# Performance work log

Measured on AMD Instinct MI355X. Metric: run time of the kernel, lower is better.

## Reference

```python
import jax, jax.numpy as jnp
import numpy as np

TEMPERATURE = 12.5      # EMDLayer temperature
SINKHORN_EPS = 0.05     # entropic regularization for the batched EMD solve
SINKHORN_ITERS = 50     # fixed iteration count (jit-friendly)
WEIGHT_EPS = 1e-05      # OpenCVSolver adds 1e-5 after relu


def setup_inputs() -> dict:
    key = jax.random.key(0)
    k1, k2, k3 = jax.random.split(key, 3)
    E, Q, W, N = 4, 75, 5, 64
    similarity_map = jax.random.uniform(k1, (E, Q, W, N, N), dtype=jnp.float32)
    weight_1 = jax.random.uniform(k2, (E, Q, W, N), dtype=jnp.float32)
    weight_2 = jax.random.uniform(k3, (E, W, Q, N), dtype=jnp.float32)
    return {"similarity_map": similarity_map, "weight_1": weight_1, "weight_2": weight_2}


def _emd_flow(cost, a, b):
    """Batched entropic-regularized EMD (log-domain Sinkhorn).
    cost: [B, N, N]; a, b: [B, N] positive marginals (each sums to N).
    Returns flow: [B, N, N] with row sums ~a and col sums ~b."""
    logK = -cost / SINKHORN_EPS            # [B, N, N]
    log_a = jnp.log(a)
    log_b = jnp.log(b)

    def step(carry, _):
        log_u, log_v = carry
        log_u = log_a - jax.scipy.special.logsumexp(logK + log_v[:, None, :], axis=2)
        log_v = log_b - jax.scipy.special.logsumexp(logK + log_u[:, :, None], axis=1)
        return (log_u, log_v), None

    init = (jnp.zeros_like(log_a), jnp.zeros_like(log_b))
    (log_u, log_v), _ = jax.lax.scan(step, init, None, length=SINKHORN_ITERS)
    return jnp.exp(logK + log_u[:, :, None] + log_v[:, None, :])


def reference(similarity_map, weight_1, weight_2):
    E, Q, W, N, _ = similarity_map.shape
    sim = similarity_map.reshape(-1, N, N)                       # [B, N, N]
    w1 = weight_1.reshape(-1, N)                                  # [B, N]
    w2 = jnp.transpose(weight_2, (0, 2, 1, 3)).reshape(-1, N)     # transpose(1,2) then flatten

    # OpenCVSolver weight preprocessing: relu + eps, renormalize to sum N
    w1 = jax.nn.relu(w1) + WEIGHT_EPS
    w1 = w1 * (N / jnp.sum(w1, axis=1, keepdims=True))
    w2 = jax.nn.relu(w2) + WEIGHT_EPS
    w2 = w2 * (N / jnp.sum(w2, axis=1, keepdims=True))

    cost = 1.0 - sim
    flow = _emd_flow(cost, w1, w2)                                # [B, N, N]
    scores = jnp.sum(flow * sim, axis=(-1, -2)).reshape(E, Q, W)
    return scores * (TEMPERATURE / N)
```

## Files before the change

kernel.cpp:

```cpp
#include <hip/hip_runtime.h>

#define N 64
#define NPAD 65
#define ITERS 50
#define TEMP 12.5f
#define WEPS 1e-5f
#define QDIM 75
#define WDIM 5

#define ROL(x) __int_as_float(__builtin_amdgcn_update_dpp(0, __float_as_int(x), 0x134, 0xF, 0xF, true))
#define ROR(x) __int_as_float(__builtin_amdgcn_update_dpp(0, __float_as_int(x), 0x13C, 0xF, 0xF, true))

__device__ __forceinline__ float waveReduceSum(float x) {
#pragma unroll
    for (int off = 32; off; off >>= 1) x += __shfl_xor(x, off, 64);
    return x;
}

__global__ __launch_bounds__(64, 1) void emd_systolic(
    const float* __restrict__ sim,
    const float* __restrict__ w1,
    const float* __restrict__ w2,
    float* __restrict__ out,
    int B)
{
    __shared__ float S[N * NPAD];

    const int lane = threadIdx.x;
    const int b    = blockIdx.x;
    const float* gm = sim + (size_t)b * N * N;

    const int dl = (__builtin_amdgcn_update_dpp(0, lane, 0x134, 0xF, 0xF, true) - lane) & 63;
    const int dr = (__builtin_amdgcn_update_dpp(0, lane, 0x13C, 0xF, 0xF, true) - lane) & 63;

    const float4* g4 = (const float4*)gm;
#pragma unroll
    for (int t = 0; t < 16; ++t) {
        float4 x = g4[t * 64 + lane];
        int idx = t * 64 + lane;
        int r = idx >> 4;
        int c = (idx & 15) * 4;
        S[r * NPAD + c + 0] = x.x;
        S[r * NPAD + c + 1] = x.y;
        S[r * NPAD + c + 2] = x.z;
        S[r * NPAD + c + 3] = x.w;
    }
    __syncthreads();

    float KL[32], KR[32], CL[32], CR[32];
#pragma unroll
    for (int m = 0; m < 32; ++m) {
        int cL = (lane + dl * m) & 63;
        int cR = (lane + dr * (m + 1)) & 63;
        KL[m] = __expf((S[lane * NPAD + cL] - 1.0f) * 20.0f);
        KR[m] = __expf((S[lane * NPAD + cR] - 1.0f) * 20.0f);
        CL[m] = __expf((S[cL * NPAD + lane] - 1.0f) * 20.0f);
        CR[m] = __expf((S[cR * NPAD + lane] - 1.0f) * 20.0f);
    }
#pragma unroll
    for (int m = 0; m < 32; ++m) {
        asm volatile("" : "+v"(KL[m]));
        asm volatile("" : "+v"(KR[m]));
        asm volatile("" : "+v"(CL[m]));
        asm volatile("" : "+v"(CR[m]));
    }

    float a_own = w1[(size_t)b * N + lane];
    a_own = fmaxf(a_own, 0.0f) + WEPS;
    a_own *= (float)N / waveReduceSum(a_own);

    const int e  = b / (QDIM * WDIM);
    const int rm = b % (QDIM * WDIM);
    const int q  = rm / WDIM, w = rm % WDIM;
    float b_own = w2[((((size_t)e * WDIM + w) * QDIM) + q) * N + lane];
    b_own = fmaxf(b_own, 0.0f) + WEPS;
    b_own *= (float)N / waveReduceSum(b_own);

    float vv = 1.0f, u = 0.0f;
#pragma unroll 1
    for (int it = 0; it < ITERS; ++it) {
        {
            float wL = vv, wR = vv;
            float accL = KL[0] * wL;
            float accR = 0.0f;
#pragma unroll
            for (int m = 1; m <= 32; ++m) {
                wR = ROR(wR);
                accR = fmaf(KR[m - 1], wR, accR);
                if (m <= 31) {
                    wL = ROL(wL);
                    accL = fmaf(KL[m], wL, accL);
                }
            }
            u = a_own * __builtin_amdgcn_rcpf(accL + accR);
        }
        {
            float wL = u, wR = u;
            float accL = CL[0] * wL;
            float accR = 0.0f;
#pragma unroll
            for (int m = 1; m <= 32; ++m) {
                wR = ROR(wR);
                accR = fmaf(CR[m - 1], wR, accR);
                if (m <= 31) {
                    wL = ROL(wL);
                    accL = fmaf(CL[m], wL, accL);
                }
            }
            vv = b_own * __builtin_amdgcn_rcpf(accL + accR);
        }
    }

    {
        const float cc = 0.69314718056f / 20.0f;
        float wL = vv, wR = vv;
        float sL = KL[0] * fmaf(__log2f(KL[0]), cc, 1.0f) * wL;
        float sR = 0.0f;
#pragma unroll
        for (int m = 1; m <= 32; ++m) {
            wR = ROR(wR);
            sR = fmaf(KR[m - 1] * fmaf(__log2f(KR[m - 1]), cc, 1.0f), wR, sR);
            if (m <= 31) {
                wL = ROL(wL);
                sL = fmaf(KL[m] * fmaf(__log2f(KL[m]), cc, 1.0f), wL, sL);
            }
        }
        float tot = waveReduceSum(u * (sL + sR));
        if (lane == 0) out[b] = tot * (TEMP / (float)N);
    }
}

extern "C" void kernel_launch(void* const* d_in, const int* in_sizes, int n_in,
                              void* d_out, int out_size, void* d_ws, size_t ws_size,
                              hipStream_t stream) {
    const float* sim = (const float*)d_in[0];
    const float* w1  = (const float*)d_in[1];
    const float* w2  = (const float*)d_in[2];
    float* out       = (float*)d_out;
    const int B = in_sizes[0] / (N * N);
    emd_systolic<<<B, 64, 0, stream>>>(sim, w1, w2, out, B);
}
```

Measured before the change: 111.5 us.

## Replace DPP systolic matvec with bf16 MFMA Sinkhorn matvecs via shared memory

Replaces the DPP-rotation register matvec in each Sinkhorn half-step with bf16 MFMA 16x16x32 operations. The kernel matrix and its transpose are held as packed bf16 fragments, and the scaling vector is broadcast through shared memory as the B operand. Only the column of the MFMA result that holds the matvec is used. Per-iteration cost shifts to MFMA issue plus LDS round trips and extra barriers. Storing the kernel matrix in bf16 lowers precision, and the final score now recomputes exp from the shared-memory similarity values.

```diff
diff --git a/kernel.cpp b/kernel.cpp
--- a/kernel.cpp
+++ b/kernel.cpp
@@ -8,8 +8,23 @@
 #define QDIM 75
 #define WDIM 5
 
-#define ROL(x) __int_as_float(__builtin_amdgcn_update_dpp(0, __float_as_int(x), 0x134, 0xF, 0xF, true))
-#define ROR(x) __int_as_float(__builtin_amdgcn_update_dpp(0, __float_as_int(x), 0x13C, 0xF, 0xF, true))
+typedef __attribute__((ext_vector_type(8))) short bf16x8;
+typedef __attribute__((ext_vector_type(4))) float f32x4;
+
+static __device__ __forceinline__ unsigned cvt_pk(float lo, float hi) {
+    unsigned r;
+    asm("v_cvt_pk_bf16_f32 %0, %1, %2" : "=v"(r) : "v"(lo), "v"(hi));
+    return r;
+}
+union FragU { unsigned u[4]; bf16x8 v; };
+static __device__ __forceinline__ bf16x8 pack8(const float e[8]) {
+    FragU f;
+    f.u[0] = cvt_pk(e[0], e[1]);
+    f.u[1] = cvt_pk(e[2], e[3]);
+    f.u[2] = cvt_pk(e[4], e[5]);
+    f.u[3] = cvt_pk(e[6], e[7]);
+    return f.v;
+}
 
 __device__ __forceinline__ float waveReduceSum(float x) {
 #pragma unroll
@@ -17,7 +32,7 @@
     return x;
 }
 
-__global__ __launch_bounds__(64, 1) void emd_systolic(
+__global__ __launch_bounds__(64, 1) void emd_mfma(
     const float* __restrict__ sim,
     const float* __restrict__ w1,
     const float* __restrict__ w2,
@@ -25,13 +40,13 @@
     int B)
 {
     __shared__ float S[N * NPAD];
+    __shared__ __align__(16) float SUM[N], U[N], V[N];
 
     const int lane = threadIdx.x;
     const int b    = blockIdx.x;
+    const int q    = lane >> 4;
+    const int m    = lane & 15;
     const float* gm = sim + (size_t)b * N * N;
-
-    const int dl = (__builtin_amdgcn_update_dpp(0, lane, 0x134, 0xF, 0xF, true) - lane) & 63;
-    const int dr = (__builtin_amdgcn_update_dpp(0, lane, 0x13C, 0xF, 0xF, true) - lane) & 63;
 
     const float4* g4 = (const float4*)gm;
 #pragma unroll
@@ -47,85 +62,112 @@
     }
     __syncthreads();
 
-    float KL[32], KR[32], CL[32], CR[32];
+    bf16x8 KA[4][2], KT[4][2];
 #pragma unroll
-    for (int m = 0; m < 32; ++m) {
-        int cL = (lane + dl * m) & 63;
-        int cR = (lane + dr * (m + 1)) & 63;
-        KL[m] = __expf((S[lane * NPAD + cL] - 1.0f) * 20.0f);
-        KR[m] = __expf((S[lane * NPAD + cR] - 1.0f) * 20.0f);
-        CL[m] = __expf((S[cL * NPAD + lane] - 1.0f) * 20.0f);
-        CR[m] = __expf((S[cR * NPAD + lane] - 1.0f) * 20.0f);
-    }
+    for (int rb = 0; rb < 4; ++rb)
 #pragma unroll
-    for (int m = 0; m < 32; ++m) {
-        asm volatile("" : "+v"(KL[m]));
-        asm volatile("" : "+v"(KR[m]));
-        asm volatile("" : "+v"(CL[m]));
-        asm volatile("" : "+v"(CR[m]));
-    }
+        for (int c = 0; c < 2; ++c) {
+            float e[8];
+            const float* p = &S[(16 * rb + m) * NPAD + 32 * c + 8 * q];
+#pragma unroll
+            for (int j = 0; j < 8; ++j) e[j] = __expf((p[j] - 1.0f) * 20.0f);
+            KA[rb][c] = pack8(e);
+#pragma unroll
+            for (int j = 0; j < 8; ++j)
+                e[j] = __expf((S[(32 * c + 8 * q + j) * NPAD + 16 * rb + m] - 1.0f) * 20.0f);
+            KT[rb][c] = pack8(e);
+        }
+#pragma unroll
+    for (int rb = 0; rb < 4; ++rb)
+#pragma unroll
+        for (int c = 0; c < 2; ++c) {
+            asm volatile("" : "+v"(KA[rb][c]));
+            asm volatile("" : "+v"(KT[rb][c]));
+        }
 
     float a_own = w1[(size_t)b * N + lane];
     a_own = fmaxf(a_own, 0.0f) + WEPS;
     a_own *= (float)N / waveReduceSum(a_own);
 
-    const int e  = b / (QDIM * WDIM);
-    const int rm = b % (QDIM * WDIM);
-    const int q  = rm / WDIM, w = rm % WDIM;
-    float b_own = w2[((((size_t)e * WDIM + w) * QDIM) + q) * N + lane];
+    const int e_  = b / (QDIM * WDIM);
+    const int rm  = b % (QDIM * WDIM);
+    const int qq  = rm / WDIM, w = rm % WDIM;
+    float b_own = w2[((((size_t)e_ * WDIM + w) * QDIM) + qq) * N + lane];
     b_own = fmaxf(b_own, 0.0f) + WEPS;
     b_own *= (float)N / waveReduceSum(b_own);
 
-    float vv = 1.0f, u = 0.0f;
+    V[lane] = 1.0f;
+    __syncthreads();
+
+    float u_own = 0.0f;
 #pragma unroll 1
     for (int it = 0; it < ITERS; ++it) {
         {
-            float wL = vv, wR = vv;
-            float accL = KL[0] * wL;
-            float accR = 0.0f;
+            const float4* p0 = (const float4*)&V[8 * q];
+            const float4* p1 = (const float4*)&V[32 + 8 * q];
+            float4 x0 = p0[0], x1 = p0[1], y0 = p1[0], y1 = p1[1];
+            float e0[8] = {x0.x, x0.y, x0.z, x0.w, x1.x, x1.y, x1.z, x1.w};
+            float e1[8] = {y0.x, y0.y, y0.z, y0.w, y1.x, y1.y, y1.z, y1.w};
+            bf16x8 B0 = pack8(e0), B1 = pack8(e1);
+            f32x4 acc[4];
 #pragma unroll
-            for (int m = 1; m <= 32; ++m) {
-                wR = ROR(wR);
-                accR = fmaf(KR[m - 1], wR, accR);
-                if (m <= 31) {
-                    wL = ROL(wL);
-                    accL = fmaf(KL[m], wL, accL);
-                }
+            for (int rb = 0; rb < 4; ++rb)
+                acc[rb] = __builtin_amdgcn_mfma_f32_16x16x32_bf16(KA[rb][1], B1, (f32x4){0.f, 0.f, 0.f, 0.f}, 0, 0, 0);
+#pragma unroll
+            for (int rb = 0; rb < 4; ++rb)
+                acc[rb] = __builtin_amdgcn_mfma_f32_16x16x32_bf16(KA[rb][0], B0, acc[rb], 0, 0, 0);
+            if (m == 0) {
+#pragma unroll
+                for (int rb = 0; rb < 4; ++rb)
+                    *(f32x4*)&SUM[16 * rb + 4 * q] = acc[rb];
             }
-            u = a_own * __builtin_amdgcn_rcpf(accL + accR);
         }
+        __syncthreads();
+        u_own = a_own * __builtin_amdgcn_rcpf(SUM[lane]);
+        U[lane] = u_own;
+        __syncthreads();
+
         {
-            float wL = u, wR = u;
-            float accL = CL[0] * wL;
-            float accR = 0.0f;
+            const float4* p0 = (const float4*)&U[8 * q];
+            const float4* p1 = (const float4*)&U[32 + 8 * q];
+            float4 x0 = p0[0], x1 = p0[1], y0 = p1[0], y1 = p1[1];
+            float e0[8] = {x0.x, x0.y, x0.z, x0.w, x1.x, x1.y, x1.z, x1.w};
+            float e1[8] = {y0.x, y0.y, y0.z, y0.w, y1.x, y1.y, y1.z, y1.w};
+            bf16x8 B0 = pack8(e0), B1 = pack8(e1);
+            f32x4 acc[4];
 #pragma unroll
-            for (int m = 1; m <= 32; ++m) {
-                wR = ROR(wR);
-                accR = fmaf(CR[m - 1], wR, accR);
-                if (m <= 31) {
-                    wL = ROL(wL);
-                    accL = fmaf(CL[m], wL, accL);
-                }
+            for (int rb = 0; rb < 4; ++rb)
+                acc[rb] = __builtin_amdgcn_mfma_f32_16x16x32_bf16(KT[rb][1], B1, (f32x4){0.f, 0.f, 0.f, 0.f}, 0, 0, 0);
+#pragma unroll
+            for (int rb = 0; rb < 4; ++rb)
+                acc[rb] = __builtin_amdgcn_mfma_f32_16x16x32_bf16(KT[rb][0], B0, acc[rb], 0, 0, 0);
+            if (m == 0) {
+#pragma unroll
+                for (int rb = 0; rb < 4; ++rb)
+                    *(f32x4*)&SUM[16 * rb + 4 * q] = acc[rb];
             }
-            vv = b_own * __builtin_amdgcn_rcpf(accL + accR);
         }
+        __syncthreads();
+        V[lane] = b_own * __builtin_amdgcn_rcpf(SUM[lane]);
+        __syncthreads();
     }
 
     {
-        const float cc = 0.69314718056f / 20.0f;
-        float wL = vv, wR = vv;
-        float sL = KL[0] * fmaf(__log2f(KL[0]), cc, 1.0f) * wL;
-        float sR = 0.0f;
+        float p0 = 0, p1 = 0;
 #pragma unroll
-        for (int m = 1; m <= 32; ++m) {
-            wR = ROR(wR);
-            sR = fmaf(KR[m - 1] * fmaf(__log2f(KR[m - 1]), cc, 1.0f), wR, sR);
-            if (m <= 31) {
-                wL = ROL(wL);
-                sL = fmaf(KL[m] * fmaf(__log2f(KL[m]), cc, 1.0f), wL, sL);
-            }
+        for (int j4 = 0; j4 < 16; ++j4) {
+            float4 vv = *(const float4*)&V[4 * j4];
+            float4 ss = *(const float4*)&S[lane * NPAD + 4 * j4];
+            float k0 = __expf((ss.x - 1.0f) * 20.0f);
+            float k1 = __expf((ss.y - 1.0f) * 20.0f);
+            float k2 = __expf((ss.z - 1.0f) * 20.0f);
+            float k3 = __expf((ss.w - 1.0f) * 20.0f);
+            p0 = fmaf(k0 * ss.x, vv.x, p0);
+            p1 = fmaf(k1 * ss.y, vv.y, p1);
+            p0 = fmaf(k2 * ss.z, vv.z, p0);
+            p1 = fmaf(k3 * ss.w, vv.w, p1);
         }
-        float tot = waveReduceSum(u * (sL + sR));
+        float tot = waveReduceSum(u_own * (p0 + p1));
         if (lane == 0) out[b] = tot * (TEMP / (float)N);
     }
 }
@@ -138,5 +180,5 @@
     const float* w2  = (const float*)d_in[2];
     float* out       = (float*)d_out;
     const int B = in_sizes[0] / (N * N);
-    emd_systolic<<<B, 64, 0, stream>>>(sim, w1, w2, out, B);
+    emd_mfma<<<B, 64, 0, stream>>>(sim, w1, w2, out, B);
 }
```

Result: faster. 108.8 us (-2.4%).
